# Performance work log

Hardware: AMD Instinct MI355X
Metric: run time of the kernel (lower is better)

The kernel has to match this reference:

```python
import jax, jax.numpy as jnp
import numpy as np

B, IN, OUT, LUT_SIZE = 32, 8192, 16384, 256


def setup_inputs() -> dict:
    key = jax.random.key(0)
    k1, k2, k3 = jax.random.split(key, 3)
    x = jax.random.normal(k1, (B, IN), dtype=jnp.float32)
    # int8 weight codes, stored as indices in [0, 256) into the dequant LUT
    weight_idx = jax.random.randint(k2, (OUT, IN), 0, LUT_SIZE, dtype=jnp.int32)
    # symmetric uniform dequant levels: code c -> (c - 128) * scale
    scale = jnp.float32(0.05 / 128.0)
    lut = (jnp.arange(LUT_SIZE, dtype=jnp.float32) - 128.0) * scale  # [256]
    bias = jax.random.normal(k3, (OUT,), dtype=jnp.float32) * 0.02
    return {"x": x, "lut": lut, "bias": bias, "weight_idx": weight_idx}


def reference(x, lut, bias, weight_idx):
    # LUT dequantization: gather fp32 weight values from the 256-entry table
    W = lut[weight_idx]                      # [OUT, IN] fp32
    # y = x @ W^T + b   (einsum: b=batch tokens, i=in_features, o=out_features)
    return jnp.einsum("bi,oi->bo", x, W) + bias  # [B, OUT]
```

## Files before the change

### kernel.cpp

```cpp
#include <hip/hip_runtime.h>

#define IN_F   8192
#define OUT_F  16384
#define BATCH  32
#define KT     1024
#define NT     (IN_F / KT)
#define PITCH  1040

typedef __attribute__((ext_vector_type(8))) short  bf16x8;
typedef __attribute__((ext_vector_type(4))) float  f32x4;

__device__ __forceinline__ unsigned f2bf(float f) {
    unsigned u = __builtin_bit_cast(unsigned, f);
    return (u + 0x7fffu + ((u >> 16) & 1u)) >> 16;
}

__device__ __forceinline__ unsigned pk_ff(float fa, float fb) {
    unsigned ua = __builtin_bit_cast(unsigned, fa);
    unsigned ub = __builtin_bit_cast(unsigned, fb);
#if __has_builtin(__builtin_amdgcn_perm)
    return __builtin_amdgcn_perm(ub, ua, 0x07060302u);
#else
    return (ua >> 16) | (ub & 0xffff0000u);
#endif
}

__device__ __forceinline__ void async_copy16(const void* g, void* l) {
    __builtin_amdgcn_global_load_lds(
        (const __attribute__((address_space(1))) unsigned*)g,
        (__attribute__((address_space(3))) unsigned*)l,
        16, 0, 0);
}

__global__ __launch_bounds__(256) void prep_kernel(
        const float* __restrict__ x, const float* __restrict__ lut,
        unsigned short* __restrict__ xbf, float* __restrict__ sumx) {
    const int b = blockIdx.x;
    const int t = threadIdx.x;
    const float s = lut[129];
    const float4* xr = (const float4*)(x + b * IN_F);
    ushort4* xo = (ushort4*)(xbf + b * IN_F);
    float acc = 0.f;
    #pragma unroll
    for (int i = 0; i < IN_F / 4 / 256; ++i) {
        float4 v = xr[t + i * 256];
        acc += v.x + v.y + v.z + v.w;
        ushort4 o;
        o.x = (unsigned short)f2bf(v.x * s);
        o.y = (unsigned short)f2bf(v.y * s);
        o.z = (unsigned short)f2bf(v.z * s);
        o.w = (unsigned short)f2bf(v.w * s);
        xo[t + i * 256] = o;
    }
    __shared__ float red[256];
    red[t] = acc;
    __syncthreads();
    for (int off = 128; off > 0; off >>= 1) {
        if (t < off) red[t] += red[t + off];
        __syncthreads();
    }
    if (t == 0) sumx[b] = red[0];
}

__global__ __launch_bounds__(256) void pack_kernel(
        const int* __restrict__ widx, unsigned char* __restrict__ wpk) {
    const long g  = (long)blockIdx.x * 256 + threadIdx.x;
    const long i0 = g * 16;
    const int  n  = (int)(i0 >> 13);
    const int  k  = (int)(i0 & 8191);
    const int  b  = n >> 4;
    const int  r  = n & 15;
    const int  t  = k >> 10;
    const int  k0 = k & 1023;
    const int4* src = (const int4*)(widx + i0);
    unsigned tmp[4];
    #pragma unroll
    for (int q = 0; q < 4; ++q) {
        int4 c = src[q];
        tmp[q] = (c.x & 255) | ((c.y & 255) << 8) |
                 ((c.z & 255) << 16) | ((unsigned)(c.w & 255) << 24);
    }
    uint4 o = {tmp[0], tmp[1], tmp[2], tmp[3]};
    *(uint4*)(wpk + (((long)(b * NT + t) * 16 + r) << 10) + k0) = o;
}

__global__ __launch_bounds__(256, 4) void gemm_kernel(
        const unsigned short* __restrict__ xbf,
        const unsigned char* __restrict__ wpk,
        const float* __restrict__ bias,
        const float* __restrict__ lut,
        const float* __restrict__ sumx,
        float* __restrict__ out) {
    __shared__ char ltile[2][16 * PITCH];
    const int tid   = threadIdx.x;
    const int wave  = tid >> 6;
    const int lane  = tid & 63;
    const int col16 = lane & 15;
    const int quad  = lane >> 4;
    const int n0    = blockIdx.x * 16;

    const unsigned char* slab = wpk + ((long)blockIdx.x * NT) * (16 * KT);
    const unsigned short* xp0 = xbf + col16 * IN_F + quad * 8;
    const unsigned short* xp1 = xp0 + 16 * IN_F;

    f32x4 acc0 = {0.f, 0.f, 0.f, 0.f};
    f32x4 acc1 = {0.f, 0.f, 0.f, 0.f};

    #define STAGE(tt, bb)                                                     \
        _Pragma("unroll")                                                     \
        for (int j = 0; j < 4; ++j) {                                         \
            const int r_ = wave * 4 + j;                                      \
            async_copy16(slab + ((long)(tt) * 16 + r_) * KT + lane * 16,      \
                         &ltile[bb][r_ * PITCH]);                             \
        }

    STAGE(0, 0)
    for (int t = 0; t < NT; ++t) {
        if (t < NT - 1) {
            STAGE(t + 1, (t + 1) & 1)
            asm volatile("s_waitcnt vmcnt(4)" ::: "memory");
        } else {
            asm volatile("s_waitcnt vmcnt(0)" ::: "memory");
        }
        asm volatile("s_barrier" ::: "memory");
        const char* base = &ltile[t & 1][col16 * PITCH + wave * 256 + quad * 8];
        #pragma unroll
        for (int s = 0; s < 8; ++s) {
            unsigned p0 = *(const unsigned*)(base + s * 32);
            unsigned p1 = *(const unsigned*)(base + s * 32 + 4);
            const int ka = t * KT + wave * 256 + s * 32;
            bf16x8 a0 = *(const bf16x8*)(xp0 + ka);
            bf16x8 a1 = *(const bf16x8*)(xp1 + ka);
            float f0 = (float)(p0 & 255u),         f1 = (float)((p0 >> 8) & 255u);
            float f2 = (float)((p0 >> 16) & 255u), f3 = (float)(p0 >> 24);
            float f4 = (float)(p1 & 255u),         f5 = (float)((p1 >> 8) & 255u);
            float f6 = (float)((p1 >> 16) & 255u), f7 = (float)(p1 >> 24);
            union { unsigned u[4]; bf16x8 v; } bB;
            bB.u[0] = pk_ff(f0, f1);
            bB.u[1] = pk_ff(f2, f3);
            bB.u[2] = pk_ff(f4, f5);
            bB.u[3] = pk_ff(f6, f7);
            acc0 = __builtin_amdgcn_mfma_f32_16x16x32_bf16(a0, bB.v, acc0, 0, 0, 0);
            acc1 = __builtin_amdgcn_mfma_f32_16x16x32_bf16(a1, bB.v, acc1, 0, 0, 0);
        }
        asm volatile("s_barrier" ::: "memory");
    }

    float* red = (float*)ltile;
    #pragma unroll
    for (int r = 0; r < 4; ++r) {
        red[wave * 512 + (quad * 4 + r)      * 16 + col16] = acc0[r];
        red[wave * 512 + (quad * 4 + r + 16) * 16 + col16] = acc1[r];
    }
    __syncthreads();
    const float l0 = lut[0];
    #pragma unroll
    for (int e0 = 0; e0 < 2; ++e0) {
        const int e = tid + e0 * 256;
        float v = red[e] + red[e + 512] + red[e + 1024] + red[e + 1536];
        const int m  = e >> 4;
        const int nn = e & 15;
        v += bias[n0 + nn] + l0 * sumx[m];
        out[(long)m * OUT_F + n0 + nn] = v;
    }
}

extern "C" void kernel_launch(void* const* d_in, const int* in_sizes, int n_in,
                              void* d_out, int out_size, void* d_ws, size_t ws_size,
                              hipStream_t stream) {
    const float* x    = (const float*)d_in[0];
    const float* lut  = (const float*)d_in[1];
    const float* bias = (const float*)d_in[2];
    const int*   widx = (const int*)d_in[3];
    float* out = (float*)d_out;

    unsigned short* xbf = (unsigned short*)d_ws;
    float* sumx = (float*)((char*)d_ws + BATCH * IN_F * 2);
    unsigned char* wpk = (unsigned char*)d_ws + (1 << 20);

    prep_kernel<<<BATCH, 256, 0, stream>>>(x, lut, xbf, sumx);
    pack_kernel<<<(long)OUT_F * IN_F / 16 / 256, 256, 0, stream>>>(widx, wpk);
    gemm_kernel<<<OUT_F / 16, 256, 0, stream>>>(xbf, wpk, bias, lut, sumx, out);
}
```

Baseline: 765.6 us.

## Pack weight codes in natural row-major layout with a coalesced looped pack kernel

```diff
diff --git a/kernel.cpp b/kernel.cpp
--- a/kernel.cpp
+++ b/kernel.cpp
@@ -23,6 +23,11 @@
 #else
     return (ua >> 16) | (ub & 0xffff0000u);
 #endif
+}
+
+__device__ __forceinline__ unsigned p4(int4 c) {
+    return (c.x & 255) | ((c.y & 255) << 8) |
+           ((c.z & 255) << 16) | ((unsigned)(c.w & 255) << 24);
 }
 
 __device__ __forceinline__ void async_copy16(const void* g, void* l) {
@@ -64,24 +69,20 @@
 
 __global__ __launch_bounds__(256) void pack_kernel(
         const int* __restrict__ widx, unsigned char* __restrict__ wpk) {
-    const long g  = (long)blockIdx.x * 256 + threadIdx.x;
-    const long i0 = g * 16;
-    const int  n  = (int)(i0 >> 13);
-    const int  k  = (int)(i0 & 8191);
-    const int  b  = n >> 4;
-    const int  r  = n & 15;
-    const int  t  = k >> 10;
-    const int  k0 = k & 1023;
-    const int4* src = (const int4*)(widx + i0);
-    unsigned tmp[4];
-    #pragma unroll
-    for (int q = 0; q < 4; ++q) {
-        int4 c = src[q];
-        tmp[q] = (c.x & 255) | ((c.y & 255) << 8) |
-                 ((c.z & 255) << 16) | ((unsigned)(c.w & 255) << 24);
+    const int tid = threadIdx.x;
+    const long base = (long)blockIdx.x * (8 * IN_F);
+    const int4* s4 = (const int4*)(widx + base);
+    unsigned*   dd = (unsigned*)(wpk + base);
+    #pragma unroll 2
+    for (int it = 0; it < 16; ++it) {
+        int4 c[4];
+        #pragma unroll
+        for (int q = 0; q < 4; ++q)
+            c[q] = s4[it * 1024 + q * 256 + tid];
+        #pragma unroll
+        for (int q = 0; q < 4; ++q)
+            dd[it * 1024 + q * 256 + tid] = p4(c[q]);
     }
-    uint4 o = {tmp[0], tmp[1], tmp[2], tmp[3]};
-    *(uint4*)(wpk + (((long)(b * NT + t) * 16 + r) << 10) + k0) = o;
 }
 
 __global__ __launch_bounds__(256, 4) void gemm_kernel(
@@ -99,7 +100,7 @@
     const int quad  = lane >> 4;
     const int n0    = blockIdx.x * 16;
 
-    const unsigned char* slab = wpk + ((long)blockIdx.x * NT) * (16 * KT);
+    const unsigned char* slab = wpk + (long)n0 * IN_F;
     const unsigned short* xp0 = xbf + col16 * IN_F + quad * 8;
     const unsigned short* xp1 = xp0 + 16 * IN_F;
 
@@ -110,7 +111,7 @@
         _Pragma("unroll")                                                     \
         for (int j = 0; j < 4; ++j) {                                         \
             const int r_ = wave * 4 + j;                                      \
-            async_copy16(slab + ((long)(tt) * 16 + r_) * KT + lane * 16,      \
+            async_copy16(slab + (long)r_ * IN_F + (tt) * KT + lane * 16,      \
                          &ltile[bb][r_ * PITCH]);                             \
         }
 
@@ -179,6 +180,6 @@
     unsigned char* wpk = (unsigned char*)d_ws + (1 << 20);
 
     prep_kernel<<<BATCH, 256, 0, stream>>>(x, lut, xbf, sumx);
-    pack_kernel<<<(long)OUT_F * IN_F / 16 / 256, 256, 0, stream>>>(widx, wpk);
+    pack_kernel<<<OUT_F / 8, 256, 0, stream>>>(widx, wpk);
     gemm_kernel<<<OUT_F / 16, 256, 0, stream>>>(xbf, wpk, bias, lut, sumx, out);
 }
```

Measured after the change: 775.0 us. About the same (+1.2%).
